# Optimization experiments

Measured on AMD Instinct MI355X. Metric: run time of the kernel, lower is better.

## Reference

```python
import jax, jax.numpy as jnp
import numpy as np

N_NODES = 50000
N_EDGES = 1600000
IN_CH = 32
HID = 64
EPS = 1e-12


def setup_inputs() -> dict:
    key = jax.random.key(0)
    ks = jax.random.split(key, 10)
    x = jax.random.normal(ks[0], (N_NODES, IN_CH), dtype=jnp.float32)
    edge_index = jax.random.randint(ks[1], (2, N_EDGES), 0, N_NODES, dtype=jnp.int64)

    def lin(k, fan_in, fan_out):
        bound = 1.0 / np.sqrt(fan_in)
        return jax.random.uniform(k, (fan_in, fan_out), jnp.float32, -bound, bound)

    params = {
        # SAGEConv layer 0: lin_l (aggregated neighbors, with bias), lin_r (root, no bias)
        'Wl0': lin(ks[2], IN_CH, HID), 'b0': jnp.zeros((HID,), jnp.float32),
        'Wr0': lin(ks[3], IN_CH, HID),
        # SAGEConv layer 1
        'Wl1': lin(ks[4], HID, HID), 'b1': jnp.zeros((HID,), jnp.float32),
        'Wr1': lin(ks[5], HID, HID),
        # classifier: Linear(64,32) -> ReLU -> Linear(32,1)
        'Wc1': lin(ks[6], HID, HID // 2), 'bc1': jnp.zeros((HID // 2,), jnp.float32),
        'Wc2': lin(ks[7], HID // 2, 1), 'bc2': jnp.zeros((1,), jnp.float32),
    }
    return {'x': x, 'edge_index': edge_index, **params}


def _sage_conv(x, src, dst, Wl, Wr, b):
    # gather messages from source nodes, mean-aggregate at destination
    msg = x[src]                                            # [E, C]
    agg = jax.ops.segment_sum(msg, dst, num_segments=N_NODES)
    cnt = jax.ops.segment_sum(jnp.ones((src.shape[0], 1), x.dtype), dst,
                              num_segments=N_NODES)
    mean = agg / jnp.maximum(cnt, 1.0)                      # [N, C]
    out = mean @ Wl + x @ Wr + b                            # [N, H]
    # normalize=True -> L2 row-normalization (F.normalize, eps=1e-12)
    nrm = jnp.linalg.norm(out, axis=-1, keepdims=True)
    return out / jnp.maximum(nrm, EPS)


def reference(x, edge_index, Wl0, b0, Wr0, Wl1, b1, Wr1, Wc1, bc1, Wc2, bc2):
    src, dst = edge_index[0], edge_index[1]
    h = _sage_conv(x, src, dst, Wl0, Wr0, b0)
    h = jax.nn.relu(h)                                      # dropout inactive (eval)
    h = _sage_conv(h, src, dst, Wl1, Wr1, b1)
    h = jax.nn.relu(h @ Wc1 + bc1)
    logits = (h @ Wc2 + bc2).squeeze(-1)                    # [N]
    return logits
```

## Files before the change

kernel.cpp:

```cpp
#include <hip/hip_runtime.h>

static constexpr int N_NODES = 50000;
static constexpr int N_EDGES = 1600000;
static constexpr int CIN = 32;
static constexpr int HID = 64;
static constexpr int NTB = N_NODES / 16;
static constexpr int NBUCK = (N_NODES + 31) / 32;
static constexpr int NB_BLD = 128;
static constexpr int EPB2 = N_EDGES / NB_BLD;

__device__ __forceinline__ unsigned short f2bf(float f) {
    unsigned int u = __float_as_uint(f);
    u = (u + 0x7fffu + ((u >> 16) & 1u)) >> 16;
    return (unsigned short)u;
}
__device__ __forceinline__ float bfhi(unsigned int u) { return __uint_as_float(u & 0xffff0000u); }
__device__ __forceinline__ float bflo(unsigned int u) { return __uint_as_float(u << 16); }

__global__ void __launch_bounds__(256)
xcast_kernel(const float* __restrict__ x, unsigned short* __restrict__ xb) {
    const int i = blockIdx.x * 256 + threadIdx.x;
    if (i < N_NODES * CIN / 4) {
        const float4 v = reinterpret_cast<const float4*>(x)[i];
        uint2 o;
        o.x = (unsigned)f2bf(v.x) | ((unsigned)f2bf(v.y) << 16);
        o.y = (unsigned)f2bf(v.z) | ((unsigned)f2bf(v.w) << 16);
        reinterpret_cast<uint2*>(xb)[i] = o;
    }
}


__global__ void __launch_bounds__(256)
histB_kernel(const int* __restrict__ ei, int* __restrict__ part) {
    __shared__ int hist[NBUCK];
    for (int i = threadIdx.x; i < NBUCK; i += 256) hist[i] = 0;
    __syncthreads();
    const int base = blockIdx.x * EPB2;
    const int t = threadIdx.x;
    for (int i0 = 0; i0 < EPB2; i0 += 1024) {
        int d[4];
#pragma unroll
        for (int k = 0; k < 4; ++k) {
            const int i = i0 + k * 256 + t;
            d[k] = (i < EPB2) ? ei[N_EDGES + base + i] : -1;
        }
#pragma unroll
        for (int k = 0; k < 4; ++k)
            if (d[k] >= 0) atomicAdd(&hist[d[k] >> 5], 1);
    }
    __syncthreads();
    for (int i = threadIdx.x; i < NBUCK; i += 256)
        part[i * NB_BLD + blockIdx.x] = hist[i];
}

__global__ void __launch_bounds__(NB_BLD)
scanA_kernel(int* __restrict__ part, int* __restrict__ btot) {
    __shared__ int s[NB_BLD];
    const int t = threadIdx.x;
    const int v = part[blockIdx.x * NB_BLD + t];
    s[t] = v;
    __syncthreads();
    for (int st = 1; st < NB_BLD; st <<= 1) {
        int u = (t >= st) ? s[t - st] : 0;
        __syncthreads();
        s[t] += u;
        __syncthreads();
    }
    part[blockIdx.x * NB_BLD + t] = s[t] - v;
    if (t == NB_BLD - 1) btot[blockIdx.x] = s[NB_BLD - 1];
}

__global__ void __launch_bounds__(1024)
scanB_kernel(const int* __restrict__ btot, int* __restrict__ bstart) {
    __shared__ int pairs[1024];
    __shared__ int v0s[1024];
    const int t = threadIdx.x;
    const int i0 = 2 * t, i1 = 2 * t + 1;
    const int v0 = (i0 < NBUCK) ? btot[i0] : 0;
    const int v1 = (i1 < NBUCK) ? btot[i1] : 0;
    v0s[t] = v0;
    const int p = v0 + v1;
    pairs[t] = p;
    __syncthreads();
    for (int st = 1; st < 1024; st <<= 1) {
        int u = (t >= st) ? pairs[t - st] : 0;
        __syncthreads();
        pairs[t] += u;
        __syncthreads();
    }
    const int base = pairs[t] - p;
    if (i0 < NBUCK) bstart[i0] = base;
    if (i1 < NBUCK) bstart[i1] = base + v0s[t];
    if (t == 1023) bstart[NBUCK] = pairs[1023];
}

__global__ void __launch_bounds__(256)
scatterB_kernel(const int* __restrict__ ei, const int* __restrict__ part,
                const int* __restrict__ bstart, unsigned* __restrict__ bentry) {
    __shared__ int cur[NBUCK];
    for (int i = threadIdx.x; i < NBUCK; i += 256)
        cur[i] = bstart[i] + part[i * NB_BLD + blockIdx.x];
    __syncthreads();
    const int base = blockIdx.x * EPB2;
    const int t = threadIdx.x;
    for (int i0 = 0; i0 < EPB2; i0 += 1024) {
        int s[4], d[4];
#pragma unroll
        for (int k = 0; k < 4; ++k) {
            const int i = i0 + k * 256 + t;
            const bool val = i < EPB2;
            s[k] = val ? ei[base + i] : 0;
            d[k] = val ? ei[N_EDGES + base + i] : -1;
        }
#pragma unroll
        for (int k = 0; k < 4; ++k)
            if (d[k] >= 0) {
                const int pos = atomicAdd(&cur[d[k] >> 5], 1);
                bentry[pos] = ((unsigned)s[k] << 5) | (unsigned)(d[k] & 31);
            }
    }
}

__global__ void __launch_bounds__(256)
sortW_kernel(const unsigned* __restrict__ bentry, const int* __restrict__ bstart,
             int* __restrict__ sorted_src, int* __restrict__ off) {
    __shared__ int cnt[32];
    __shared__ int base[33];
    __shared__ int cur[32];
    const int b = blockIdx.x, t = threadIdx.x;
    const int s0 = bstart[b], s1 = bstart[b + 1];
    if (t < 32) cnt[t] = 0;
    __syncthreads();
    for (int i = s0 + t; i < s1; i += 256)
        atomicAdd(&cnt[bentry[i] & 31], 1);
    __syncthreads();
    if (t == 0) {
        int run = s0;
#pragma unroll
        for (int l = 0; l < 32; ++l) { base[l] = run; cur[l] = run; run += cnt[l]; }
        base[32] = run;
    }
    __syncthreads();
    if (t <= 32) {
        const int gn = b * 32 + t;
        if (gn <= N_NODES) off[gn] = base[t];
    }
    for (int i = s0 + t; i < s1; i += 256) {
        const unsigned e = bentry[i];
        const int pos = atomicAdd(&cur[e & 31], 1);
        sorted_src[pos] = (int)(e >> 5);
    }
}

__global__ void __launch_bounds__(256)
agg0_kernel(const unsigned short* __restrict__ xb,
            const int* __restrict__ off, const int* __restrict__ src,
            unsigned short* __restrict__ mean0b) {
    const int node = blockIdx.x * 4 + (threadIdx.x >> 6);
    const int lane = threadIdx.x & 63;
    if (node >= N_NODES) return;
    const int e0 = off[node], e1 = off[node + 1];
    const int deg = e1 - e0;
    const int grp = lane >> 3, cg = lane & 7;

    float a[4] = {0, 0, 0, 0};
    for (int base = e0; base < e1; base += 64) {
        const int cnt = min(64, e1 - base);
        const int p = base + lane;
        const int sidx = (p < e1) ? src[p] : 0;
        const int nb = (cnt + 7) >> 3;
        uint2 u[8];
#pragma unroll
        for (int t = 0; t < 8; ++t) u[t] = make_uint2(0u, 0u);
#pragma unroll
        for (int t = 0; t < 8; ++t) {
            if (t < nb) {
                const int pos = (t << 3) | grp;
                const int s = __shfl(sidx, pos);
                if (pos < cnt)
                    u[t] = *reinterpret_cast<const uint2*>(xb + (size_t)s * 32 + cg * 4);
            }
        }
#pragma unroll
        for (int t = 0; t < 8; ++t) {
            a[0] += bflo(u[t].x); a[1] += bfhi(u[t].x);
            a[2] += bflo(u[t].y); a[3] += bfhi(u[t].y);
        }
    }
#pragma unroll
    for (int j = 0; j < 4; ++j) {
        a[j] += __shfl_xor(a[j], 8);
        a[j] += __shfl_xor(a[j], 16);
        a[j] += __shfl_xor(a[j], 32);
    }
    const float inv = 1.0f / fmaxf((float)deg, 1.0f);
    if (grp == 0) {
        uint2 o;
        o.x = (unsigned)f2bf(a[0] * inv) | ((unsigned)f2bf(a[1] * inv) << 16);
        o.y = (unsigned)f2bf(a[2] * inv) | ((unsigned)f2bf(a[3] * inv) << 16);
        reinterpret_cast<uint2*>(mean0b)[node * 8 + cg] = o;
    }
}

__global__ void __launch_bounds__(256)
agg1p_kernel(const unsigned short* __restrict__ tbl,
             const int* __restrict__ off, const int* __restrict__ src,
             float* __restrict__ dstbase) {
    const int node = blockIdx.x * 4 + (threadIdx.x >> 6);
    const int lane = threadIdx.x & 63;
    if (node >= N_NODES) return;
    const int e0 = off[node], e1 = off[node + 1];
    const int deg = e1 - e0;
    const int grp = lane >> 3, cg = lane & 7;

    float a[4] = {0, 0, 0, 0};
    for (int base = e0; base < e1; base += 64) {
        const int cnt = min(64, e1 - base);
        const int p = base + lane;
        const int sidx = (p < e1) ? src[p] : 0;
        const int nb = (cnt + 7) >> 3;
        uint2 u[8];
#pragma unroll
        for (int t = 0; t < 8; ++t) u[t] = make_uint2(0u, 0u);
#pragma unroll
        for (int t = 0; t < 8; ++t) {
            if (t < nb) {
                const int pos = (t << 3) | grp;
                const int s = __shfl(sidx, pos);
                if (pos < cnt)
                    u[t] = *reinterpret_cast<const uint2*>(tbl + (size_t)s * 32 + cg * 4);
            }
        }
#pragma unroll
        for (int t = 0; t < 8; ++t) {
            a[0] += bflo(u[t].x); a[1] += bfhi(u[t].x);
            a[2] += bflo(u[t].y); a[3] += bfhi(u[t].y);
        }
    }
#pragma unroll
    for (int j = 0; j < 4; ++j) {
        a[j] += __shfl_xor(a[j], 8);
        a[j] += __shfl_xor(a[j], 16);
        a[j] += __shfl_xor(a[j], 32);
    }
    const float inv = 1.0f / fmaxf((float)deg, 1.0f);
    if (grp == 0) {
        float4 o = make_float4(a[0] * inv, a[1] * inv, a[2] * inv, a[3] * inv);
        *reinterpret_cast<float4*>(dstbase + (size_t)node * HID + cg * 4) = o;
    }
}

__global__ void __launch_bounds__(256)
transform0_kernel(const float* __restrict__ x,
                  const unsigned short* __restrict__ mean0b,
                  const float* __restrict__ Wl0, const float* __restrict__ Wr0,
                  const float* __restrict__ b0,
                  unsigned short* __restrict__ hbA,
                  unsigned short* __restrict__ hbB) {
    __shared__ float sWl[CIN * HID];
    __shared__ float sWr[CIN * HID];
    __shared__ float sMin[16 * CIN];
    __shared__ float sXin[16 * CIN];
    const int t = threadIdx.x;
    const int blk = blockIdx.x;
    reinterpret_cast<float4*>(sWl)[t]       = reinterpret_cast<const float4*>(Wl0)[t];
    reinterpret_cast<float4*>(sWl)[t + 256] = reinterpret_cast<const float4*>(Wl0)[t + 256];
    reinterpret_cast<float4*>(sWr)[t]       = reinterpret_cast<const float4*>(Wr0)[t];
    reinterpret_cast<float4*>(sWr)[t + 256] = reinterpret_cast<const float4*>(Wr0)[t + 256];
    {
        const unsigned u = reinterpret_cast<const unsigned*>(mean0b)[blk * 256 + t];
        sMin[2 * t]     = bflo(u);
        sMin[2 * t + 1] = bfhi(u);
    }
    if (t < 128)
        reinterpret_cast<float4*>(sXin)[t] =
            reinterpret_cast<const float4*>(x + (size_t)blk * 16 * CIN)[t];
    __syncthreads();

    const int n = t >> 4, cg = t & 15;
    const float4 bv = reinterpret_cast<const float4*>(b0)[cg];
    float a[4] = {bv.x, bv.y, bv.z, bv.w};
#pragma unroll
    for (int k = 0; k < CIN; ++k) {
        const float m  = sMin[n * CIN + k];
        const float xx = sXin[n * CIN + k];
        const float4 wl = reinterpret_cast<const float4*>(sWl + k * HID)[cg];
        const float4 wr = reinterpret_cast<const float4*>(sWr + k * HID)[cg];
        a[0] = fmaf(m, wl.x, fmaf(xx, wr.x, a[0]));
        a[1] = fmaf(m, wl.y, fmaf(xx, wr.y, a[1]));
        a[2] = fmaf(m, wl.z, fmaf(xx, wr.z, a[2]));
        a[3] = fmaf(m, wl.w, fmaf(xx, wr.w, a[3]));
    }
    float ss = a[0] * a[0] + a[1] * a[1] + a[2] * a[2] + a[3] * a[3];
    ss += __shfl_xor(ss, 1);
    ss += __shfl_xor(ss, 2);
    ss += __shfl_xor(ss, 4);
    ss += __shfl_xor(ss, 8);
    const float sc = 1.0f / fmaxf(sqrtf(ss), 1e-12f);
    uint2 o;
    o.x = (unsigned)f2bf(fmaxf(a[0] * sc, 0.f)) | ((unsigned)f2bf(fmaxf(a[1] * sc, 0.f)) << 16);
    o.y = (unsigned)f2bf(fmaxf(a[2] * sc, 0.f)) | ((unsigned)f2bf(fmaxf(a[3] * sc, 0.f)) << 16);
    const int g = blk * 16 + n;
    unsigned short* dst = (cg < 8) ? hbA : hbB;
    reinterpret_cast<uint2*>(dst)[(size_t)g * 8 + (cg & 7)] = o;
}

__global__ void __launch_bounds__(256)
transform1_kernel(const unsigned short* __restrict__ hbA,
                  const unsigned short* __restrict__ hbB,
                  const float* __restrict__ mean1f,
                  const float* __restrict__ Wl1, const float* __restrict__ Wr1,
                  const float* __restrict__ b1,
                  const float* __restrict__ Wc1, const float* __restrict__ bc1,
                  const float* __restrict__ Wc2, const float* __restrict__ bc2,
                  float* __restrict__ out) {
    __shared__ float sWl[HID * HID];
    __shared__ float sWr[HID * HID];
    __shared__ float sWc[HID * 32];
    __shared__ float sMin[16 * HID];
    __shared__ float sHin[16 * HID];
    __shared__ float sV[16 * HID];
    const int t = threadIdx.x;
    const int blk = blockIdx.x;
#pragma unroll
    for (int i = 0; i < 4; ++i) {
        reinterpret_cast<float4*>(sWl)[t + 256 * i] = reinterpret_cast<const float4*>(Wl1)[t + 256 * i];
        reinterpret_cast<float4*>(sWr)[t + 256 * i] = reinterpret_cast<const float4*>(Wr1)[t + 256 * i];
    }
#pragma unroll
    for (int i = 0; i < 2; ++i)
        reinterpret_cast<float4*>(sWc)[t + 256 * i] = reinterpret_cast<const float4*>(Wc1)[t + 256 * i];
    reinterpret_cast<float4*>(sMin)[t] =
        reinterpret_cast<const float4*>(mean1f + (size_t)blk * 16 * HID)[t];
    {
        const int g = blk * 16 + (t >> 4);
        const int sub = t & 15;
        const unsigned short* part = (sub < 8) ? hbA : hbB;
        const uint2 hu = reinterpret_cast<const uint2*>(part)[(size_t)g * 8 + (sub & 7)];
        sHin[4 * t]     = bflo(hu.x);
        sHin[4 * t + 1] = bfhi(hu.x);
        sHin[4 * t + 2] = bflo(hu.y);
        sHin[4 * t + 3] = bfhi(hu.y);
    }
    __syncthreads();

    const int n = t >> 4, cg = t & 15;
    const float4 bv = reinterpret_cast<const float4*>(b1)[cg];
    float a[4] = {bv.x, bv.y, bv.z, bv.w};
#pragma unroll
    for (int k = 0; k < HID; ++k) {
        const float m  = sMin[n * HID + k];
        const float hh = sHin[n * HID + k];
        const float4 wl = reinterpret_cast<const float4*>(sWl + k * HID)[cg];
        const float4 wr = reinterpret_cast<const float4*>(sWr + k * HID)[cg];
        a[0] = fmaf(m, wl.x, fmaf(hh, wr.x, a[0]));
        a[1] = fmaf(m, wl.y, fmaf(hh, wr.y, a[1]));
        a[2] = fmaf(m, wl.z, fmaf(hh, wr.z, a[2]));
        a[3] = fmaf(m, wl.w, fmaf(hh, wr.w, a[3]));
    }
    float ss = a[0] * a[0] + a[1] * a[1] + a[2] * a[2] + a[3] * a[3];
    ss += __shfl_xor(ss, 1);
    ss += __shfl_xor(ss, 2);
    ss += __shfl_xor(ss, 4);
    ss += __shfl_xor(ss, 8);
    const float sc = 1.0f / fmaxf(sqrtf(ss), 1e-12f);
    sV[n * HID + 4 * cg + 0] = a[0] * sc;
    sV[n * HID + 4 * cg + 1] = a[1] * sc;
    sV[n * HID + 4 * cg + 2] = a[2] * sc;
    sV[n * HID + 4 * cg + 3] = a[3] * sc;
    __syncthreads();

    float c1a = bc1[cg], c1b = bc1[cg + 16];
#pragma unroll
    for (int k = 0; k < HID; ++k) {
        const float vv = sV[n * HID + k];
        c1a = fmaf(vv, sWc[k * 32 + cg], c1a);
        c1b = fmaf(vv, sWc[k * 32 + cg + 16], c1b);
    }
    float pp = fmaxf(c1a, 0.f) * Wc2[cg] + fmaxf(c1b, 0.f) * Wc2[cg + 16];
    pp += __shfl_xor(pp, 1);
    pp += __shfl_xor(pp, 2);
    pp += __shfl_xor(pp, 4);
    pp += __shfl_xor(pp, 8);
    if (cg == 0) out[blk * 16 + n] = pp + bc2[0];
}

extern "C" void kernel_launch(void* const* d_in, const int* in_sizes, int n_in,
                              void* d_out, int out_size, void* d_ws, size_t ws_size,
                              hipStream_t stream) {
    const float* x   = (const float*)d_in[0];
    const int*   ei  = (const int*)d_in[1];
    const float* Wl0 = (const float*)d_in[2];
    const float* b0  = (const float*)d_in[3];
    const float* Wr0 = (const float*)d_in[4];
    const float* Wl1 = (const float*)d_in[5];
    const float* b1  = (const float*)d_in[6];
    const float* Wr1 = (const float*)d_in[7];
    const float* Wc1 = (const float*)d_in[8];
    const float* bc1 = (const float*)d_in[9];
    const float* Wc2 = (const float*)d_in[10];
    const float* bc2 = (const float*)d_in[11];
    float* out = (float*)d_out;

    float* W = (float*)d_ws;
    int*            part   = (int*)W;
    int*            btot   = (int*)(W + 200064);
    int*            bstart = (int*)(W + 201632);
    unsigned*       bentry = (unsigned*)(W + 1600000);
    unsigned short* mean0b = (unsigned short*)W;
    float*          mean1f = W;
    int*            sorted_src = (int*)(W + 3200000);
    int*            off    = (int*)(W + 4800000);
    unsigned short* hbA    = (unsigned short*)(W + 4850016);
    unsigned short* hbB    = (unsigned short*)(W + 5650016);
    unsigned short* xb     = (unsigned short*)(W + 6450016);

    const int T = 256;
    xcast_kernel<<<(N_NODES * CIN / 4 + T - 1) / T, T, 0, stream>>>(x, xb);
    histB_kernel<<<NB_BLD, T, 0, stream>>>(ei, part);
    scanA_kernel<<<NBUCK, NB_BLD, 0, stream>>>(part, btot);
    scanB_kernel<<<1, 1024, 0, stream>>>(btot, bstart);
    scatterB_kernel<<<NB_BLD, T, 0, stream>>>(ei, part, bstart, bentry);
    sortW_kernel<<<NBUCK, T, 0, stream>>>(bentry, bstart, sorted_src, off);

    const int ngrid = (N_NODES + 3) / 4;
    agg0_kernel<<<ngrid, T, 0, stream>>>(xb, off, sorted_src, mean0b);
    transform0_kernel<<<NTB, T, 0, stream>>>(x, mean0b, Wl0, Wr0, b0, hbA, hbB);
    agg1p_kernel<<<ngrid, T, 0, stream>>>(hbA, off, sorted_src, mean1f);
    agg1p_kernel<<<ngrid, T, 0, stream>>>(hbB, off, sorted_src, mean1f + 32);
    transform1_kernel<<<NTB, T, 0, stream>>>(hbA, hbB, mean1f, Wl1, Wr1, b1,
                                             Wc1, bc1, Wc2, bc2, out);
}
```

Measured before the change: 169.0 us.

## Rewrite SAGE transform kernels as wave-per-16-nodes with register-resident weights

Both dense transform kernels now assign 16 nodes to each wavefront, keep weight columns in per-lane registers, and broadcast input features via readlane instead of staging everything through shared memory. This removes the per-block LDS loads of weights and the block barriers. In exchange it raises register pressure (especially in transform1 with ~160 weight registers) and serialises the nodes within a wave, which may lower occupancy.

```diff
diff --git a/kernel.cpp b/kernel.cpp
--- a/kernel.cpp
+++ b/kernel.cpp
@@ -4,7 +4,6 @@
 static constexpr int N_EDGES = 1600000;
 static constexpr int CIN = 32;
 static constexpr int HID = 64;
-static constexpr int NTB = N_NODES / 16;
 static constexpr int NBUCK = (N_NODES + 31) / 32;
 static constexpr int NB_BLD = 128;
 static constexpr int EPB2 = N_EDGES / NB_BLD;
@@ -14,8 +13,14 @@
     u = (u + 0x7fffu + ((u >> 16) & 1u)) >> 16;
     return (unsigned short)u;
 }
+__device__ __forceinline__ float bf2f(unsigned short u) {
+    return __uint_as_float(((unsigned)u) << 16);
+}
 __device__ __forceinline__ float bfhi(unsigned int u) { return __uint_as_float(u & 0xffff0000u); }
 __device__ __forceinline__ float bflo(unsigned int u) { return __uint_as_float(u << 16); }
+__device__ __forceinline__ float rl(float v, int k) {
+    return __int_as_float(__builtin_amdgcn_readlane(__float_as_int(v), k));
+}
 
 __global__ void __launch_bounds__(256)
 xcast_kernel(const float* __restrict__ x, unsigned short* __restrict__ xb) {
@@ -257,52 +262,34 @@
                   const float* __restrict__ b0,
                   unsigned short* __restrict__ hbA,
                   unsigned short* __restrict__ hbB) {
-    __shared__ float sWl[CIN * HID];
-    __shared__ float sWr[CIN * HID];
-    __shared__ float sMin[16 * CIN];
-    __shared__ float sXin[16 * CIN];
-    const int t = threadIdx.x;
-    const int blk = blockIdx.x;
-    reinterpret_cast<float4*>(sWl)[t]       = reinterpret_cast<const float4*>(Wl0)[t];
-    reinterpret_cast<float4*>(sWl)[t + 256] = reinterpret_cast<const float4*>(Wl0)[t + 256];
-    reinterpret_cast<float4*>(sWr)[t]       = reinterpret_cast<const float4*>(Wr0)[t];
-    reinterpret_cast<float4*>(sWr)[t + 256] = reinterpret_cast<const float4*>(Wr0)[t + 256];
-    {
-        const unsigned u = reinterpret_cast<const unsigned*>(mean0b)[blk * 256 + t];
-        sMin[2 * t]     = bflo(u);
-        sMin[2 * t + 1] = bfhi(u);
-    }
-    if (t < 128)
-        reinterpret_cast<float4*>(sXin)[t] =
-            reinterpret_cast<const float4*>(x + (size_t)blk * 16 * CIN)[t];
-    __syncthreads();
-
-    const int n = t >> 4, cg = t & 15;
-    const float4 bv = reinterpret_cast<const float4*>(b0)[cg];
-    float a[4] = {bv.x, bv.y, bv.z, bv.w};
-#pragma unroll
-    for (int k = 0; k < CIN; ++k) {
-        const float m  = sMin[n * CIN + k];
-        const float xx = sXin[n * CIN + k];
-        const float4 wl = reinterpret_cast<const float4*>(sWl + k * HID)[cg];
-        const float4 wr = reinterpret_cast<const float4*>(sWr + k * HID)[cg];
-        a[0] = fmaf(m, wl.x, fmaf(xx, wr.x, a[0]));
-        a[1] = fmaf(m, wl.y, fmaf(xx, wr.y, a[1]));
-        a[2] = fmaf(m, wl.z, fmaf(xx, wr.z, a[2]));
-        a[3] = fmaf(m, wl.w, fmaf(xx, wr.w, a[3]));
-    }
-    float ss = a[0] * a[0] + a[1] * a[1] + a[2] * a[2] + a[3] * a[3];
-    ss += __shfl_xor(ss, 1);
-    ss += __shfl_xor(ss, 2);
-    ss += __shfl_xor(ss, 4);
-    ss += __shfl_xor(ss, 8);
-    const float sc = 1.0f / fmaxf(sqrtf(ss), 1e-12f);
-    uint2 o;
-    o.x = (unsigned)f2bf(fmaxf(a[0] * sc, 0.f)) | ((unsigned)f2bf(fmaxf(a[1] * sc, 0.f)) << 16);
-    o.y = (unsigned)f2bf(fmaxf(a[2] * sc, 0.f)) | ((unsigned)f2bf(fmaxf(a[3] * sc, 0.f)) << 16);
-    const int g = blk * 16 + n;
-    unsigned short* dst = (cg < 8) ? hbA : hbB;
-    reinterpret_cast<uint2*>(dst)[(size_t)g * 8 + (cg & 7)] = o;
+    const int lane = threadIdx.x & 63;
+    const int wv = blockIdx.x * 4 + (threadIdx.x >> 6);
+    float wl[CIN], wr[CIN];
+#pragma unroll
+    for (int k = 0; k < CIN; ++k) wl[k] = Wl0[k * HID + lane];
+#pragma unroll
+    for (int k = 0; k < CIN; ++k) wr[k] = Wr0[k * HID + lane];
+    const float bias = b0[lane];
+    const int lk = lane & 31;
+    const int n0 = wv * 16;
+    const int n1 = min(n0 + 16, N_NODES);
+    for (int n = n0; n < n1; ++n) {
+        const float mreg = bf2f(mean0b[(size_t)n * CIN + lk]);
+        const float xreg = x[(size_t)n * CIN + lk];
+        float accA = 0.f, accB = 0.f;
+#pragma unroll
+        for (int k = 0; k < CIN; ++k) {
+            accA = fmaf(rl(mreg, k), wl[k], accA);
+            accB = fmaf(rl(xreg, k), wr[k], accB);
+        }
+        float o = accA + accB + bias;
+        float ss = o * o;
+#pragma unroll
+        for (int m = 32; m > 0; m >>= 1) ss += __shfl_xor(ss, m);
+        const float v = fmaxf(o / fmaxf(sqrtf(ss), 1e-12f), 0.0f);
+        unsigned short* dst = (lane < 32) ? hbA : hbB;
+        dst[(size_t)n * 32 + lk] = f2bf(v);
+    }
 }
 
 __global__ void __launch_bounds__(256)
@@ -314,75 +301,54 @@
                   const float* __restrict__ Wc1, const float* __restrict__ bc1,
                   const float* __restrict__ Wc2, const float* __restrict__ bc2,
                   float* __restrict__ out) {
-    __shared__ float sWl[HID * HID];
-    __shared__ float sWr[HID * HID];
-    __shared__ float sWc[HID * 32];
-    __shared__ float sMin[16 * HID];
-    __shared__ float sHin[16 * HID];
-    __shared__ float sV[16 * HID];
-    const int t = threadIdx.x;
-    const int blk = blockIdx.x;
-#pragma unroll
-    for (int i = 0; i < 4; ++i) {
-        reinterpret_cast<float4*>(sWl)[t + 256 * i] = reinterpret_cast<const float4*>(Wl1)[t + 256 * i];
-        reinterpret_cast<float4*>(sWr)[t + 256 * i] = reinterpret_cast<const float4*>(Wr1)[t + 256 * i];
-    }
-#pragma unroll
-    for (int i = 0; i < 2; ++i)
-        reinterpret_cast<float4*>(sWc)[t + 256 * i] = reinterpret_cast<const float4*>(Wc1)[t + 256 * i];
-    reinterpret_cast<float4*>(sMin)[t] =
-        reinterpret_cast<const float4*>(mean1f + (size_t)blk * 16 * HID)[t];
-    {
-        const int g = blk * 16 + (t >> 4);
-        const int sub = t & 15;
-        const unsigned short* part = (sub < 8) ? hbA : hbB;
-        const uint2 hu = reinterpret_cast<const uint2*>(part)[(size_t)g * 8 + (sub & 7)];
-        sHin[4 * t]     = bflo(hu.x);
-        sHin[4 * t + 1] = bfhi(hu.x);
-        sHin[4 * t + 2] = bflo(hu.y);
-        sHin[4 * t + 3] = bfhi(hu.y);
-    }
-    __syncthreads();
-
-    const int n = t >> 4, cg = t & 15;
-    const float4 bv = reinterpret_cast<const float4*>(b1)[cg];
-    float a[4] = {bv.x, bv.y, bv.z, bv.w};
-#pragma unroll
-    for (int k = 0; k < HID; ++k) {
-        const float m  = sMin[n * HID + k];
-        const float hh = sHin[n * HID + k];
-        const float4 wl = reinterpret_cast<const float4*>(sWl + k * HID)[cg];
-        const float4 wr = reinterpret_cast<const float4*>(sWr + k * HID)[cg];
-        a[0] = fmaf(m, wl.x, fmaf(hh, wr.x, a[0]));
-        a[1] = fmaf(m, wl.y, fmaf(hh, wr.y, a[1]));
-        a[2] = fmaf(m, wl.z, fmaf(hh, wr.z, a[2]));
-        a[3] = fmaf(m, wl.w, fmaf(hh, wr.w, a[3]));
-    }
-    float ss = a[0] * a[0] + a[1] * a[1] + a[2] * a[2] + a[3] * a[3];
-    ss += __shfl_xor(ss, 1);
-    ss += __shfl_xor(ss, 2);
-    ss += __shfl_xor(ss, 4);
-    ss += __shfl_xor(ss, 8);
-    const float sc = 1.0f / fmaxf(sqrtf(ss), 1e-12f);
-    sV[n * HID + 4 * cg + 0] = a[0] * sc;
-    sV[n * HID + 4 * cg + 1] = a[1] * sc;
-    sV[n * HID + 4 * cg + 2] = a[2] * sc;
-    sV[n * HID + 4 * cg + 3] = a[3] * sc;
-    __syncthreads();
-
-    float c1a = bc1[cg], c1b = bc1[cg + 16];
-#pragma unroll
-    for (int k = 0; k < HID; ++k) {
-        const float vv = sV[n * HID + k];
-        c1a = fmaf(vv, sWc[k * 32 + cg], c1a);
-        c1b = fmaf(vv, sWc[k * 32 + cg + 16], c1b);
-    }
-    float pp = fmaxf(c1a, 0.f) * Wc2[cg] + fmaxf(c1b, 0.f) * Wc2[cg + 16];
-    pp += __shfl_xor(pp, 1);
-    pp += __shfl_xor(pp, 2);
-    pp += __shfl_xor(pp, 4);
-    pp += __shfl_xor(pp, 8);
-    if (cg == 0) out[blk * 16 + n] = pp + bc2[0];
+    const int lane = threadIdx.x & 63;
+    const int wv = blockIdx.x * 4 + (threadIdx.x >> 6);
+    float wl[HID], wr[HID];
+#pragma unroll
+    for (int k = 0; k < HID; ++k) wl[k] = Wl1[k * HID + lane];
+#pragma unroll
+    for (int k = 0; k < HID; ++k) wr[k] = Wr1[k * HID + lane];
+    const int j = lane & 31, kh = lane >> 5;
+    float wc[32];
+#pragma unroll
+    for (int i = 0; i < 32; ++i) wc[i] = Wc1[(kh * 32 + i) * 32 + j];
+    const float bias = b1[lane];
+    const float c0 = bc1[j];
+    const float w2 = Wc2[j];
+    const float bb = bc2[0];
+    const int n0 = wv * 16;
+    const int n1 = min(n0 + 16, N_NODES);
+    for (int n = n0; n < n1; ++n) {
+        const float mreg = mean1f[(size_t)n * HID + lane];
+        const unsigned short* htbl = (lane < 32) ? hbA : hbB;
+        const float hreg = bf2f(htbl[(size_t)n * 32 + j]);
+        float accA = 0.f, accB = 0.f;
+#pragma unroll
+        for (int k = 0; k < HID; ++k) {
+            accA = fmaf(rl(mreg, k), wl[k], accA);
+            accB = fmaf(rl(hreg, k), wr[k], accB);
+        }
+        float o = accA + accB + bias;
+        float ss = o * o;
+#pragma unroll
+        for (int m = 32; m > 0; m >>= 1) ss += __shfl_xor(ss, m);
+        const float v = o / fmaxf(sqrtf(ss), 1e-12f);
+        float c = c0;
+#pragma unroll
+        for (int i = 0; i < 32; ++i) {
+            const float vlo = rl(v, i);
+            const float vhi = rl(v, 32 + i);
+            c = fmaf(kh ? vhi : vlo, wc[i], c);
+        }
+        c += __shfl_xor(c, 32);
+        float p = fmaxf(c, 0.0f) * w2;
+        p += __shfl_xor(p, 1);
+        p += __shfl_xor(p, 2);
+        p += __shfl_xor(p, 4);
+        p += __shfl_xor(p, 8);
+        p += __shfl_xor(p, 16);
+        if (lane == 0) out[n] = p + bb;
+    }
 }
 
 extern "C" void kernel_launch(void* const* d_in, const int* in_sizes, int n_in,
@@ -424,10 +390,11 @@
     sortW_kernel<<<NBUCK, T, 0, stream>>>(bentry, bstart, sorted_src, off);
 
     const int ngrid = (N_NODES + 3) / 4;
+    const int tgrid = (N_NODES + 63) / 64;
     agg0_kernel<<<ngrid, T, 0, stream>>>(xb, off, sorted_src, mean0b);
-    transform0_kernel<<<NTB, T, 0, stream>>>(x, mean0b, Wl0, Wr0, b0, hbA, hbB);
+    transform0_kernel<<<tgrid, T, 0, stream>>>(x, mean0b, Wl0, Wr0, b0, hbA, hbB);
     agg1p_kernel<<<ngrid, T, 0, stream>>>(hbA, off, sorted_src, mean1f);
     agg1p_kernel<<<ngrid, T, 0, stream>>>(hbB, off, sorted_src, mean1f + 32);
-    transform1_kernel<<<NTB, T, 0, stream>>>(hbA, hbB, mean1f, Wl1, Wr1, b1,
-                                             Wc1, bc1, Wc2, bc2, out);
-}
+    transform1_kernel<<<tgrid, T, 0, stream>>>(hbA, hbB, mean1f, Wl1, Wr1, b1,
+                                               Wc1, bc1, Wc2, bc2, out);
+}
```

New measurement: 224.1 us. 32.6% more time.

## Process 64 nodes per block in transform kernels with register-blocked weights

Applied to the files above, without the earlier changes.

Both dense transform kernels now handle 64 nodes per block instead of 16. Each thread loads weight float4s from shared memory once per 4-wide k-chunk and reuses them across 4 nodes, reading node inputs straight from global memory instead of staging them in shared memory. This amortizes the per-block weight staging, which is especially large in transform1 at about 40KB, over four times as many nodes. The classifier stage is rewritten to compute 8 outputs per thread from a padded shared buffer. The cost is more registers and a tail guard for the last partial block.

```diff
diff --git a/kernel.cpp b/kernel.cpp
--- a/kernel.cpp
+++ b/kernel.cpp
@@ -4,15 +4,18 @@
 static constexpr int N_EDGES = 1600000;
 static constexpr int CIN = 32;
 static constexpr int HID = 64;
-static constexpr int NTB = N_NODES / 16;
 static constexpr int NBUCK = (N_NODES + 31) / 32;
 static constexpr int NB_BLD = 128;
 static constexpr int EPB2 = N_EDGES / NB_BLD;
+static constexpr int NTB2 = (N_NODES + 63) / 64;
 
 __device__ __forceinline__ unsigned short f2bf(float f) {
     unsigned int u = __float_as_uint(f);
     u = (u + 0x7fffu + ((u >> 16) & 1u)) >> 16;
     return (unsigned short)u;
+}
+__device__ __forceinline__ float bf2f(unsigned short u) {
+    return __uint_as_float(((unsigned)u) << 16);
 }
 __device__ __forceinline__ float bfhi(unsigned int u) { return __uint_as_float(u & 0xffff0000u); }
 __device__ __forceinline__ float bflo(unsigned int u) { return __uint_as_float(u << 16); }
@@ -259,52 +262,70 @@
                   unsigned short* __restrict__ hbB) {
     __shared__ float sWl[CIN * HID];
     __shared__ float sWr[CIN * HID];
-    __shared__ float sMin[16 * CIN];
-    __shared__ float sXin[16 * CIN];
-    const int t = threadIdx.x;
-    const int blk = blockIdx.x;
+    const int t = threadIdx.x;
     reinterpret_cast<float4*>(sWl)[t]       = reinterpret_cast<const float4*>(Wl0)[t];
     reinterpret_cast<float4*>(sWl)[t + 256] = reinterpret_cast<const float4*>(Wl0)[t + 256];
     reinterpret_cast<float4*>(sWr)[t]       = reinterpret_cast<const float4*>(Wr0)[t];
     reinterpret_cast<float4*>(sWr)[t + 256] = reinterpret_cast<const float4*>(Wr0)[t + 256];
-    {
-        const unsigned u = reinterpret_cast<const unsigned*>(mean0b)[blk * 256 + t];
-        sMin[2 * t]     = bflo(u);
-        sMin[2 * t + 1] = bfhi(u);
-    }
-    if (t < 128)
-        reinterpret_cast<float4*>(sXin)[t] =
-            reinterpret_cast<const float4*>(x + (size_t)blk * 16 * CIN)[t];
-    __syncthreads();
-
-    const int n = t >> 4, cg = t & 15;
+    __syncthreads();
+
+    const int lane = t & 63, wid = t >> 6;
+    const int cg = lane & 15, rep = lane >> 4;
+    const int nbase = blockIdx.x * 64 + wid * 16 + rep;
     const float4 bv = reinterpret_cast<const float4*>(b0)[cg];
-    float a[4] = {bv.x, bv.y, bv.z, bv.w};
-#pragma unroll
-    for (int k = 0; k < CIN; ++k) {
-        const float m  = sMin[n * CIN + k];
-        const float xx = sXin[n * CIN + k];
-        const float4 wl = reinterpret_cast<const float4*>(sWl + k * HID)[cg];
-        const float4 wr = reinterpret_cast<const float4*>(sWr + k * HID)[cg];
-        a[0] = fmaf(m, wl.x, fmaf(xx, wr.x, a[0]));
-        a[1] = fmaf(m, wl.y, fmaf(xx, wr.y, a[1]));
-        a[2] = fmaf(m, wl.z, fmaf(xx, wr.z, a[2]));
-        a[3] = fmaf(m, wl.w, fmaf(xx, wr.w, a[3]));
-    }
-    float ss = a[0] * a[0] + a[1] * a[1] + a[2] * a[2] + a[3] * a[3];
-    ss += __shfl_xor(ss, 1);
-    ss += __shfl_xor(ss, 2);
-    ss += __shfl_xor(ss, 4);
-    ss += __shfl_xor(ss, 8);
-    const float sc = 1.0f / fmaxf(sqrtf(ss), 1e-12f);
-    uint2 o;
-    o.x = (unsigned)f2bf(fmaxf(a[0] * sc, 0.f)) | ((unsigned)f2bf(fmaxf(a[1] * sc, 0.f)) << 16);
-    o.y = (unsigned)f2bf(fmaxf(a[2] * sc, 0.f)) | ((unsigned)f2bf(fmaxf(a[3] * sc, 0.f)) << 16);
-    const int g = blk * 16 + n;
-    unsigned short* dst = (cg < 8) ? hbA : hbB;
-    reinterpret_cast<uint2*>(dst)[(size_t)g * 8 + (cg & 7)] = o;
-}
-
+    float acc[4][4];
+#pragma unroll
+    for (int s = 0; s < 4; ++s) {
+        acc[s][0] = bv.x; acc[s][1] = bv.y; acc[s][2] = bv.z; acc[s][3] = bv.w;
+    }
+    for (int kc = 0; kc < CIN; kc += 4) {
+        float4 wl4[4], wr4[4];
+#pragma unroll
+        for (int kk = 0; kk < 4; ++kk) {
+            wl4[kk] = *reinterpret_cast<const float4*>(sWl + (kc + kk) * HID + 4 * cg);
+            wr4[kk] = *reinterpret_cast<const float4*>(sWr + (kc + kk) * HID + 4 * cg);
+        }
+#pragma unroll
+        for (int s = 0; s < 4; ++s) {
+            const int n = nbase + 4 * s;
+            if (n < N_NODES) {
+                const uint2 mu = *reinterpret_cast<const uint2*>(mean0b + (size_t)n * CIN + kc);
+                const float4 xv = *reinterpret_cast<const float4*>(x + (size_t)n * CIN + kc);
+                const float m4[4] = {bflo(mu.x), bfhi(mu.x), bflo(mu.y), bfhi(mu.y)};
+                const float x4[4] = {xv.x, xv.y, xv.z, xv.w};
+#pragma unroll
+                for (int kk = 0; kk < 4; ++kk) {
+                    acc[s][0] = fmaf(m4[kk], wl4[kk].x, fmaf(x4[kk], wr4[kk].x, acc[s][0]));
+                    acc[s][1] = fmaf(m4[kk], wl4[kk].y, fmaf(x4[kk], wr4[kk].y, acc[s][1]));
+                    acc[s][2] = fmaf(m4[kk], wl4[kk].z, fmaf(x4[kk], wr4[kk].z, acc[s][2]));
+                    acc[s][3] = fmaf(m4[kk], wl4[kk].w, fmaf(x4[kk], wr4[kk].w, acc[s][3]));
+                }
+            }
+        }
+    }
+#pragma unroll
+    for (int s = 0; s < 4; ++s) {
+        float ss = acc[s][0] * acc[s][0] + acc[s][1] * acc[s][1] +
+                   acc[s][2] * acc[s][2] + acc[s][3] * acc[s][3];
+        ss += __shfl_xor(ss, 1);
+        ss += __shfl_xor(ss, 2);
+        ss += __shfl_xor(ss, 4);
+        ss += __shfl_xor(ss, 8);
+        const float sc = 1.0f / fmaxf(sqrtf(ss), 1e-12f);
+        const int n = nbase + 4 * s;
+        if (n < N_NODES) {
+            uint2 o;
+            o.x = (unsigned)f2bf(fmaxf(acc[s][0] * sc, 0.f)) |
+                  ((unsigned)f2bf(fmaxf(acc[s][1] * sc, 0.f)) << 16);
+            o.y = (unsigned)f2bf(fmaxf(acc[s][2] * sc, 0.f)) |
+                  ((unsigned)f2bf(fmaxf(acc[s][3] * sc, 0.f)) << 16);
+            unsigned short* dst = (cg < 8) ? hbA : hbB;
+            *reinterpret_cast<uint2*>(dst + (size_t)n * 32 + (cg & 7) * 4) = o;
+        }
+    }
+}
+
+static constexpr int SVP = 68;
 __global__ void __launch_bounds__(256)
 transform1_kernel(const unsigned short* __restrict__ hbA,
                   const unsigned short* __restrict__ hbB,
@@ -317,11 +338,8 @@
     __shared__ float sWl[HID * HID];
     __shared__ float sWr[HID * HID];
     __shared__ float sWc[HID * 32];
-    __shared__ float sMin[16 * HID];
-    __shared__ float sHin[16 * HID];
-    __shared__ float sV[16 * HID];
-    const int t = threadIdx.x;
-    const int blk = blockIdx.x;
+    __shared__ float sV[64 * SVP];
+    const int t = threadIdx.x;
 #pragma unroll
     for (int i = 0; i < 4; ++i) {
         reinterpret_cast<float4*>(sWl)[t + 256 * i] = reinterpret_cast<const float4*>(Wl1)[t + 256 * i];
@@ -330,59 +348,87 @@
 #pragma unroll
     for (int i = 0; i < 2; ++i)
         reinterpret_cast<float4*>(sWc)[t + 256 * i] = reinterpret_cast<const float4*>(Wc1)[t + 256 * i];
-    reinterpret_cast<float4*>(sMin)[t] =
-        reinterpret_cast<const float4*>(mean1f + (size_t)blk * 16 * HID)[t];
-    {
-        const int g = blk * 16 + (t >> 4);
-        const int sub = t & 15;
-        const unsigned short* part = (sub < 8) ? hbA : hbB;
-        const uint2 hu = reinterpret_cast<const uint2*>(part)[(size_t)g * 8 + (sub & 7)];
-        sHin[4 * t]     = bflo(hu.x);
-        sHin[4 * t + 1] = bfhi(hu.x);
-        sHin[4 * t + 2] = bflo(hu.y);
-        sHin[4 * t + 3] = bfhi(hu.y);
-    }
-    __syncthreads();
-
-    const int n = t >> 4, cg = t & 15;
+    __syncthreads();
+
+    const int lane = t & 63, wid = t >> 6;
+    const int cg = lane & 15, rep = lane >> 4;
+    const int nbase = blockIdx.x * 64 + wid * 16 + rep;
     const float4 bv = reinterpret_cast<const float4*>(b1)[cg];
-    float a[4] = {bv.x, bv.y, bv.z, bv.w};
-#pragma unroll
-    for (int k = 0; k < HID; ++k) {
-        const float m  = sMin[n * HID + k];
-        const float hh = sHin[n * HID + k];
-        const float4 wl = reinterpret_cast<const float4*>(sWl + k * HID)[cg];
-        const float4 wr = reinterpret_cast<const float4*>(sWr + k * HID)[cg];
-        a[0] = fmaf(m, wl.x, fmaf(hh, wr.x, a[0]));
-        a[1] = fmaf(m, wl.y, fmaf(hh, wr.y, a[1]));
-        a[2] = fmaf(m, wl.z, fmaf(hh, wr.z, a[2]));
-        a[3] = fmaf(m, wl.w, fmaf(hh, wr.w, a[3]));
-    }
-    float ss = a[0] * a[0] + a[1] * a[1] + a[2] * a[2] + a[3] * a[3];
-    ss += __shfl_xor(ss, 1);
-    ss += __shfl_xor(ss, 2);
-    ss += __shfl_xor(ss, 4);
-    ss += __shfl_xor(ss, 8);
-    const float sc = 1.0f / fmaxf(sqrtf(ss), 1e-12f);
-    sV[n * HID + 4 * cg + 0] = a[0] * sc;
-    sV[n * HID + 4 * cg + 1] = a[1] * sc;
-    sV[n * HID + 4 * cg + 2] = a[2] * sc;
-    sV[n * HID + 4 * cg + 3] = a[3] * sc;
-    __syncthreads();
-
-    float c1a = bc1[cg], c1b = bc1[cg + 16];
-#pragma unroll
-    for (int k = 0; k < HID; ++k) {
-        const float vv = sV[n * HID + k];
-        c1a = fmaf(vv, sWc[k * 32 + cg], c1a);
-        c1b = fmaf(vv, sWc[k * 32 + cg + 16], c1b);
-    }
-    float pp = fmaxf(c1a, 0.f) * Wc2[cg] + fmaxf(c1b, 0.f) * Wc2[cg + 16];
+    float acc[4][4];
+#pragma unroll
+    for (int s = 0; s < 4; ++s) {
+        acc[s][0] = bv.x; acc[s][1] = bv.y; acc[s][2] = bv.z; acc[s][3] = bv.w;
+    }
+    for (int kc = 0; kc < HID; kc += 4) {
+        float4 wl4[4], wr4[4];
+#pragma unroll
+        for (int kk = 0; kk < 4; ++kk) {
+            wl4[kk] = *reinterpret_cast<const float4*>(sWl + (kc + kk) * HID + 4 * cg);
+            wr4[kk] = *reinterpret_cast<const float4*>(sWr + (kc + kk) * HID + 4 * cg);
+        }
+        const unsigned short* htbl = (kc < 32) ? hbA : hbB;
+        const int hoff = kc & 31;
+#pragma unroll
+        for (int s = 0; s < 4; ++s) {
+            const int n = nbase + 4 * s;
+            if (n < N_NODES) {
+                const float4 mv = *reinterpret_cast<const float4*>(mean1f + (size_t)n * HID + kc);
+                const uint2 hu = *reinterpret_cast<const uint2*>(htbl + (size_t)n * 32 + hoff);
+                const float m4[4] = {mv.x, mv.y, mv.z, mv.w};
+                const float h4[4] = {bflo(hu.x), bfhi(hu.x), bflo(hu.y), bfhi(hu.y)};
+#pragma unroll
+                for (int kk = 0; kk < 4; ++kk) {
+                    acc[s][0] = fmaf(m4[kk], wl4[kk].x, fmaf(h4[kk], wr4[kk].x, acc[s][0]));
+                    acc[s][1] = fmaf(m4[kk], wl4[kk].y, fmaf(h4[kk], wr4[kk].y, acc[s][1]));
+                    acc[s][2] = fmaf(m4[kk], wl4[kk].z, fmaf(h4[kk], wr4[kk].z, acc[s][2]));
+                    acc[s][3] = fmaf(m4[kk], wl4[kk].w, fmaf(h4[kk], wr4[kk].w, acc[s][3]));
+                }
+            }
+        }
+    }
+#pragma unroll
+    for (int s = 0; s < 4; ++s) {
+        float ss = acc[s][0] * acc[s][0] + acc[s][1] * acc[s][1] +
+                   acc[s][2] * acc[s][2] + acc[s][3] * acc[s][3];
+        ss += __shfl_xor(ss, 1);
+        ss += __shfl_xor(ss, 2);
+        ss += __shfl_xor(ss, 4);
+        ss += __shfl_xor(ss, 8);
+        const float sc = 1.0f / fmaxf(sqrtf(ss), 1e-12f);
+        const int ln = wid * 16 + rep + 4 * s;
+        sV[ln * SVP + 4 * cg + 0] = acc[s][0] * sc;
+        sV[ln * SVP + 4 * cg + 1] = acc[s][1] * sc;
+        sV[ln * SVP + 4 * cg + 2] = acc[s][2] * sc;
+        sV[ln * SVP + 4 * cg + 3] = acc[s][3] * sc;
+    }
+    __syncthreads();
+
+    const int n2 = t >> 2, ig = t & 3;
+    float c1[8];
+#pragma unroll
+    for (int u = 0; u < 8; ++u) c1[u] = bc1[ig * 8 + u];
+#pragma unroll 4
+    for (int c = 0; c < HID; ++c) {
+        const float vv = sV[n2 * SVP + c];
+        const float4 w0 = *reinterpret_cast<const float4*>(sWc + c * 32 + ig * 8);
+        const float4 w1 = *reinterpret_cast<const float4*>(sWc + c * 32 + ig * 8 + 4);
+        c1[0] = fmaf(vv, w0.x, c1[0]);
+        c1[1] = fmaf(vv, w0.y, c1[1]);
+        c1[2] = fmaf(vv, w0.z, c1[2]);
+        c1[3] = fmaf(vv, w0.w, c1[3]);
+        c1[4] = fmaf(vv, w1.x, c1[4]);
+        c1[5] = fmaf(vv, w1.y, c1[5]);
+        c1[6] = fmaf(vv, w1.z, c1[6]);
+        c1[7] = fmaf(vv, w1.w, c1[7]);
+    }
+    float pp = 0.f;
+#pragma unroll
+    for (int u = 0; u < 8; ++u)
+        pp = fmaf(fmaxf(c1[u], 0.f), Wc2[ig * 8 + u], pp);
     pp += __shfl_xor(pp, 1);
     pp += __shfl_xor(pp, 2);
-    pp += __shfl_xor(pp, 4);
-    pp += __shfl_xor(pp, 8);
-    if (cg == 0) out[blk * 16 + n] = pp + bc2[0];
+    const int g = blockIdx.x * 64 + n2;
+    if (ig == 0 && g < N_NODES) out[g] = pp + bc2[0];
 }
 
 extern "C" void kernel_launch(void* const* d_in, const int* in_sizes, int n_in,
@@ -425,9 +471,9 @@
 
     const int ngrid = (N_NODES + 3) / 4;
     agg0_kernel<<<ngrid, T, 0, stream>>>(xb, off, sorted_src, mean0b);
-    transform0_kernel<<<NTB, T, 0, stream>>>(x, mean0b, Wl0, Wr0, b0, hbA, hbB);
+    transform0_kernel<<<NTB2, T, 0, stream>>>(x, mean0b, Wl0, Wr0, b0, hbA, hbB);
     agg1p_kernel<<<ngrid, T, 0, stream>>>(hbA, off, sorted_src, mean1f);
     agg1p_kernel<<<ngrid, T, 0, stream>>>(hbB, off, sorted_src, mean1f + 32);
-    transform1_kernel<<<NTB, T, 0, stream>>>(hbA, hbB, mean1f, Wl1, Wr1, b1,
-                                             Wc1, bc1, Wc2, bc2, out);
-}
+    transform1_kernel<<<NTB2, T, 0, stream>>>(hbA, hbB, mean1f, Wl1, Wr1, b1,
+                                              Wc1, bc1, Wc2, bc2, out);
+}
```

Result: no change. 172.3 us (+2.0%).
